# Kernel tuning notes

Measured on AMD Instinct MI355X. Metric: run time of the kernel, lower is better.

## Reference

```python
import jax, jax.numpy as jnp
import numpy as np

EPS = 1e-5
PATCH_HW = 4096   # 64*64
STEP = 2048


def _conv(x, w, b=None, stride=(1, 1), pad=((0, 0), (0, 0))):
    y = jax.lax.conv_general_dilated(x, w, stride, pad,
                                     dimension_numbers=('NCHW', 'OIHW', 'NCHW'))
    return y if b is None else y + b[None, :, None, None]


def _bn(x, s, b, m, v):
    # inference-mode BatchNorm2d
    inv = s * jax.lax.rsqrt(v + EPS)
    return (x - m[None, :, None, None]) * inv[None, :, None, None] + b[None, :, None, None]


def _forward(x, w1, b1, w2, b2, w3, b3,
             c5a_w, bn5a_s, bn5a_b, bn5a_m, bn5a_v,
             c5c_w, bn5c_s, bn5c_b, bn5c_m, bn5c_v,
             c51_w, bn51_s, bn51_b, bn51_m, bn51_v,
             c52_w, bn52_s, bn52_b, bn52_m, bn52_v,
             pam_q_w, pam_q_b, pam_k_w, pam_k_b, pam_v_w, pam_v_b,
             pam_gamma, cam_gamma, c8_w, c8_b):
    B, L = x.shape
    need = PATCH_HW - (L % PATCH_HW)          # torch pads even when L%hw==0; L chosen non-multiple
    xp = jnp.pad(x, ((0, 0), (0, need)))
    nw = (xp.shape[1] - PATCH_HW) // STEP + 1  # sliding windows (unfold)
    idx = jnp.arange(nw)[:, None] * STEP + jnp.arange(PATCH_HW)[None, :]
    # [nw,1,64,64].reshape(1,1,hw,nw) in torch is a pure row-major reshape
    c_in = xp[:, idx].reshape(B, 1, PATCH_HW, nw)   # [B,1,4096,61]
    # FCN backbone
    h = jax.nn.relu(_conv(c_in, w1, b1, (4, 4), ((4, 4), (4, 4))))   # [B,128,1025,16]
    h = jax.nn.relu(_conv(h, w2, b2, (2, 2), ((2, 2), (2, 2))))      # [B,256,513,8]
    h = jax.nn.relu(_conv(h, w3, b3, (1, 1), ((1, 1), (1, 1))))      # [B,128,513,8]
    p1 = ((1, 1), (1, 1))
    # PAM branch
    feat1 = jax.nn.relu(_bn(_conv(h, c5a_w, None, (1, 1), p1), bn5a_s, bn5a_b, bn5a_m, bn5a_v))
    _, C, Hh, Ww = feat1.shape
    N = Hh * Ww                                    # 4104
    q = _conv(feat1, pam_q_w, pam_q_b).reshape(B, -1, N)   # [B,4,N]
    k = _conv(feat1, pam_k_w, pam_k_b).reshape(B, -1, N)
    attn = jax.nn.softmax(jnp.einsum('bdn,bdm->bnm', q, k), axis=-1)   # [B,N,N], no scaling (as in source)
    v = _conv(feat1, pam_v_w, pam_v_b).reshape(B, C, N)
    sa = pam_gamma * jnp.einsum('bcj,bij->bci', v, attn).reshape(feat1.shape) + feat1
    sa_conv = jax.nn.relu(_bn(_conv(sa, c51_w, None, (1, 1), p1), bn51_s, bn51_b, bn51_m, bn51_v))
    # CAM branch
    feat2 = jax.nn.relu(_bn(_conv(h, c5c_w, None, (1, 1), p1), bn5c_s, bn5c_b, bn5c_m, bn5c_v))
    Xf = feat2.reshape(B, C, N)
    energy = jnp.einsum('bcn,bdn->bcd', Xf, Xf)                 # [B,C,C]
    cattn = jax.nn.softmax(jnp.max(energy, -1, keepdims=True) - energy, axis=-1)  # max-subtract inversion
    sc = cam_gamma * jnp.einsum('bcd,bdn->bcn', cattn, Xf).reshape(feat2.shape) + feat2
    sc_conv = jax.nn.relu(_bn(_conv(sc, c52_w, None, (1, 1), p1), bn52_s, bn52_b, bn52_m, bn52_v))
    # fused head output (conv8; dropout is identity in eval)
    out = _conv(sa_conv + sc_conv, c8_w, c8_b)                  # [B,nclass,513,8]
    return out[:, None]                                          # torch.stack adds a dim -> [B,1,nclass,513,8]


def setup_inputs() -> dict:
    key = jax.random.key(0)
    it = iter(jax.random.split(key, 40))
    def rn(shape, s=0.05):
        return jax.random.normal(next(it), shape, jnp.float32) * s
    d = {}
    d['x'] = jax.random.normal(next(it), (4, 126975), jnp.float32)
    d['w1'] = rn((128, 1, 8, 8));   d['b1'] = rn((128,))
    d['w2'] = rn((256, 128, 5, 5)); d['b2'] = rn((256,))
    d['w3'] = rn((128, 256, 3, 3)); d['b3'] = rn((128,))
    for tag, cin in (('5a', 128), ('5c', 128), ('51', 32), ('52', 32)):
        d['c' + tag + '_w'] = rn((32, cin, 3, 3))
        d['bn' + tag + '_s'] = jnp.ones((32,), jnp.float32)
        d['bn' + tag + '_b'] = jnp.zeros((32,), jnp.float32)
        d['bn' + tag + '_m'] = jnp.zeros((32,), jnp.float32)
        d['bn' + tag + '_v'] = jnp.ones((32,), jnp.float32)
    d['pam_q_w'] = rn((4, 32, 1, 1));  d['pam_q_b'] = rn((4,))
    d['pam_k_w'] = rn((4, 32, 1, 1));  d['pam_k_b'] = rn((4,))
    d['pam_v_w'] = rn((32, 32, 1, 1)); d['pam_v_b'] = rn((32,))
    d['pam_gamma'] = jnp.array([0.5], jnp.float32)  # nonzero so attention path is live
    d['cam_gamma'] = jnp.array([0.5], jnp.float32)
    d['c8_w'] = rn((2, 32, 1, 1)); d['c8_b'] = rn((2,))
    return d


def reference(x, w1, b1, w2, b2, w3, b3,
              c5a_w, bn5a_s, bn5a_b, bn5a_m, bn5a_v,
              c5c_w, bn5c_s, bn5c_b, bn5c_m, bn5c_v,
              c51_w, bn51_s, bn51_b, bn51_m, bn51_v,
              c52_w, bn52_s, bn52_b, bn52_m, bn52_v,
              pam_q_w, pam_q_b, pam_k_w, pam_k_b, pam_v_w, pam_v_b,
              pam_gamma, cam_gamma, c8_w, c8_b):
    return _forward(x, w1, b1, w2, b2, w3, b3,
                    c5a_w, bn5a_s, bn5a_b, bn5a_m, bn5a_v,
                    c5c_w, bn5c_s, bn5c_b, bn5c_m, bn5c_v,
                    c51_w, bn51_s, bn51_b, bn51_m, bn51_v,
                    c52_w, bn52_s, bn52_b, bn52_m, bn52_v,
                    pam_q_w, pam_q_b, pam_k_w, pam_k_b, pam_v_w, pam_v_b,
                    pam_gamma, cam_gamma, c8_w, c8_b)
```

## Files before the change

kernel.cpp:

```cpp
#include <hip/hip_runtime.h>
#include <cstddef>

constexpr int BB   = 4;
constexpr int LX   = 126975;
constexpr int H0   = 4096, W0 = 61;
constexpr int C1   = 128, H1 = 1025, W1 = 16;
constexpr int C2   = 256, H2 = 513,  W2 = 8;
constexpr int C3   = 128;
constexpr int NN   = H2 * W2;
constexpr int NSPLIT = 15;
constexpr int JSPAN  = 288;
constexpr int NPAD   = 4104;

constexpr size_t SZ_H1    = (size_t)BB * C1 * H1 * W1;
constexpr size_t SZ_P2    = (size_t)BB * C2 * NN;
constexpr size_t SZ_P3    = (size_t)BB * C3 * NN;
constexpr size_t SZ_F     = (size_t)BB * 32 * NN;
constexpr size_t SZ_QK    = (size_t)BB * 4 * NN;
constexpr size_t SZ_ACCP  = (size_t)NSPLIT * BB * 32 * NPAD;
constexpr size_t SZ_ML    = (size_t)NSPLIT * BB * 2 * NPAD;

constexpr size_t OFF_H1   = 0;
constexpr size_t OFF_P3A  = 0;
constexpr size_t OFF_P3B  = SZ_P3;
constexpr size_t OFF_ACCP = 0;
constexpr size_t OFF_ML   = OFF_ACCP + SZ_ACCP;
constexpr size_t RB       = SZ_H1;
constexpr size_t OFF_P2   = RB;
constexpr size_t OFF_F1   = RB;
constexpr size_t OFF_F2   = OFF_F1 + SZ_F;
constexpr size_t OFF_Q    = OFF_F2 + SZ_F;
constexpr size_t OFF_K    = OFF_Q  + SZ_QK;
constexpr size_t OFF_V    = OFF_K  + SZ_QK;
constexpr size_t OFF_SA   = OFF_V  + SZ_F;
constexpr size_t OFF_SC   = OFF_SA + SZ_F;
constexpr size_t OFF_EN   = RB + SZ_P2;
constexpr size_t OFF_W2T  = OFF_EN + 4096;
constexpr size_t OFF_W3T  = OFF_W2T + 819200;

__device__ __forceinline__ float frelu(float x) { return x > 0.f ? x : 0.f; }

__global__ __launch_bounds__(256) void k_wtrans(const float* __restrict__ w2,
                                                const float* __restrict__ w3,
                                                float* __restrict__ w2T,
                                                float* __restrict__ w3T) {
  const int k = blockIdx.x, oc = threadIdx.x;
  w2T[(size_t)k * 256 + oc] = w2[(size_t)oc * 3200 + k];
  if (k < 2304 && oc < 128) w3T[(size_t)k * 128 + oc] = w3[(size_t)oc * 2304 + k];
}

__global__ __launch_bounds__(256) void k_conv1(const float* __restrict__ x,
                                               const float* __restrict__ w1,
                                               const float* __restrict__ b1,
                                               float* __restrict__ h1) {
  __shared__ __align__(16) float tile[68 * 68];
  const int oh0 = blockIdx.x * 16;
  const int oc0 = blockIdx.y * 8;
  const int b   = blockIdx.z;
  const int tid = threadIdx.x;
  const int ih0 = oh0 * 4 - 4;
  for (int e = tid; e < 68 * 68; e += 256) {
    int row = e / 68, col = e - row * 68;
    int ih = ih0 + row, iw = col - 4;
    float v = 0.f;
    if (ih >= 0 && ih < H0 && iw >= 0 && iw < W0) {
      int l   = ih * W0 + iw;
      int pos = (l >> 12) * 2048 + (l & 4095);
      if (pos < LX) v = x[(size_t)b * LX + pos];
    }
    tile[e] = v;
  }
  __syncthreads();
  const int oh_l = tid >> 4, ow = tid & 15;
  float acc[8];
#pragma unroll
  for (int o = 0; o < 8; ++o) acc[o] = 0.f;
#pragma unroll
  for (int kh = 0; kh < 8; ++kh) {
    const float* rp = &tile[(4 * oh_l + kh) * 68 + 4 * ow];
    float4 a0 = *(const float4*)rp;
    float4 a1 = *(const float4*)(rp + 4);
    float r[8] = {a0.x, a0.y, a0.z, a0.w, a1.x, a1.y, a1.z, a1.w};
#pragma unroll
    for (int kw = 0; kw < 8; ++kw) {
#pragma unroll
      for (int o = 0; o < 8; ++o)
        acc[o] = fmaf(r[kw], w1[(oc0 + o) * 64 + kh * 8 + kw], acc[o]);
    }
  }
  const int oh = oh0 + oh_l;
  if (oh < H1) {
#pragma unroll
    for (int o = 0; o < 8; ++o) {
      float v = frelu(acc[o] + b1[oc0 + o]);
      h1[(((size_t)b * C1 + oc0 + o) * H1 + oh) * W1 + ow] = v;
    }
  }
}

__global__ __launch_bounds__(128) void k_conv2(const float* __restrict__ h1,
                                               const float* __restrict__ w2T,
                                               const float* __restrict__ b2,
                                               float* __restrict__ p2) {
  __shared__ __align__(16) float tin[4 * 19 * 20];
  const int oh0 = blockIdx.x * 8;
  const int oc0 = blockIdx.y * 32;
  const int b   = blockIdx.z;
  const int tid = threadIdx.x;
  const int oh_l = tid & 7, ocg = tid >> 3;
  const int ih0 = oh0 * 2 - 2;
  float acc[2][8] = {};
  for (int cc = 0; cc < 32; ++cc) {
    __syncthreads();
    for (int e = tid; e < 4 * 19 * 16; e += 128) {
      int ci = e / 304, r = e - ci * 304;
      int tr = r >> 4, c = r & 15;
      int ih = ih0 + tr;
      int cin = cc * 4 + ci;
      float v = 0.f;
      if (ih >= 0 && ih < H1) v = h1[(((size_t)b * C1 + cin) * H1 + ih) * W1 + c];
      tin[(ci * 19 + tr) * 20 + c] = v;
    }
    __syncthreads();
#pragma unroll 1
    for (int ci = 0; ci < 4; ++ci) {
      const float* wbase = &w2T[(size_t)((cc * 4 + ci) * 25) * 256 + oc0 + ocg * 2];
#pragma unroll
      for (int kh = 0; kh < 5; ++kh) {
        const float* rp = &tin[(ci * 19 + 2 * oh_l + kh) * 20];
        float4 a0 = *(const float4*)rp;
        float4 a1 = *(const float4*)(rp + 4);
        float4 a2 = *(const float4*)(rp + 8);
        float4 a3 = *(const float4*)(rp + 12);
        float rr[19];
        rr[0] = 0.f; rr[1] = 0.f; rr[18] = 0.f;
        rr[2] = a0.x; rr[3] = a0.y; rr[4] = a0.z; rr[5] = a0.w;
        rr[6] = a1.x; rr[7] = a1.y; rr[8] = a1.z; rr[9] = a1.w;
        rr[10] = a2.x; rr[11] = a2.y; rr[12] = a2.z; rr[13] = a2.w;
        rr[14] = a3.x; rr[15] = a3.y; rr[16] = a3.z; rr[17] = a3.w;
#pragma unroll
        for (int kw = 0; kw < 5; ++kw) {
          float2 wv = *(const float2*)&wbase[(kh * 5 + kw) * 256];
#pragma unroll
          for (int ow = 0; ow < 8; ++ow) {
            float r = rr[2 * ow + kw];
            acc[0][ow] = fmaf(r, wv.x, acc[0][ow]);
            acc[1][ow] = fmaf(r, wv.y, acc[1][ow]);
          }
        }
      }
    }
  }
  const int oh = oh0 + oh_l;
  if (oh < H2) {
#pragma unroll
    for (int o = 0; o < 2; ++o) {
      int oc = oc0 + ocg * 2 + o;
      float bo = b2[oc];
      float* dst = &p2[((size_t)b * C2 + oc) * NN + oh * 8];
      *(float4*)dst       = make_float4(frelu(acc[o][0] + bo), frelu(acc[o][1] + bo),
                                        frelu(acc[o][2] + bo), frelu(acc[o][3] + bo));
      *(float4*)(dst + 4) = make_float4(frelu(acc[o][4] + bo), frelu(acc[o][5] + bo),
                                        frelu(acc[o][6] + bo), frelu(acc[o][7] + bo));
    }
  }
}

__global__ __launch_bounds__(128) void k_conv3(const float* __restrict__ p2,
                                               const float* __restrict__ w3T,
                                               float* __restrict__ p3a,
                                               float* __restrict__ p3b) {
  __shared__ __align__(16) float tin[8 * 10 * 12];
  const int oh0  = blockIdx.x * 8;
  const int oc0  = (blockIdx.y & 3) * 32;
  const int half = blockIdx.y >> 2;
  const int b    = blockIdx.z;
  const int tid  = threadIdx.x;
  const int oh_l = tid & 7, ocg = tid >> 3;
  float acc[2][8] = {};
  float* outp = half ? p3b : p3a;
  for (int cc = 0; cc < 16; ++cc) {
    __syncthreads();
    for (int e = tid; e < 640; e += 128) {
      int ci = e / 80, r = e - ci * 80;
      int tr = r >> 3, c = r & 7;
      int ih = oh0 - 1 + tr;
      int cin = half * 128 + cc * 8 + ci;
      float v = 0.f;
      if (ih >= 0 && ih < H2) v = p2[((size_t)b * C2 + cin) * NN + ih * 8 + c];
      tin[(ci * 10 + tr) * 12 + c] = v;
    }
    __syncthreads();
#pragma unroll 1
    for (int ci = 0; ci < 8; ++ci) {
      const float* wbase = &w3T[(size_t)((half * 128 + cc * 8 + ci) * 9) * 128 + oc0 + ocg * 2];
#pragma unroll
      for (int kh = 0; kh < 3; ++kh) {
        const float* rp = &tin[(ci * 10 + oh_l + kh) * 12];
        float4 a0 = *(const float4*)rp;
        float4 a1 = *(const float4*)(rp + 4);
        float rr[10];
        rr[0] = 0.f; rr[9] = 0.f;
        rr[1] = a0.x; rr[2] = a0.y; rr[3] = a0.z; rr[4] = a0.w;
        rr[5] = a1.x; rr[6] = a1.y; rr[7] = a1.z; rr[8] = a1.w;
#pragma unroll
        for (int kw = 0; kw < 3; ++kw) {
          float2 wv = *(const float2*)&wbase[(kh * 3 + kw) * 128];
#pragma unroll
          for (int ow = 0; ow < 8; ++ow) {
            float r = rr[ow + kw];
            acc[0][ow] = fmaf(r, wv.x, acc[0][ow]);
            acc[1][ow] = fmaf(r, wv.y, acc[1][ow]);
          }
        }
      }
    }
  }
  const int oh = oh0 + oh_l;
  if (oh < H2) {
#pragma unroll
    for (int o = 0; o < 2; ++o) {
      int oc = oc0 + ocg * 2 + o;
      float* dst = &outp[((size_t)b * C3 + oc) * NN + oh * 8];
      *(float4*)dst       = make_float4(acc[o][0], acc[o][1], acc[o][2], acc[o][3]);
      *(float4*)(dst + 4) = make_float4(acc[o][4], acc[o][5], acc[o][6], acc[o][7]);
    }
  }
}

__global__ __launch_bounds__(128) void k_c5(const float* __restrict__ p3a,
                                            const float* __restrict__ p3b,
                                            const float* __restrict__ b3,
                                            const float* __restrict__ wa,
                                            const float* __restrict__ sa5, const float* __restrict__ ba5,
                                            const float* __restrict__ ma5, const float* __restrict__ va5,
                                            const float* __restrict__ wc,
                                            const float* __restrict__ sc5, const float* __restrict__ bc5,
                                            const float* __restrict__ mc5, const float* __restrict__ vc5,
                                            float* __restrict__ f1, float* __restrict__ f2) {
  __shared__ __align__(16) float tin[8 * 10 * 12];
  __shared__ __align__(16) float twt[72 * 64];
  const int oh0 = blockIdx.x * 8;
  const int b   = blockIdx.y;
  const int tid = threadIdx.x;
  const int vocg = tid >> 3, oh_l = tid & 7;
  float acc[4][8] = {};
  for (int cc = 0; cc < 16; ++cc) {
    __syncthreads();
    for (int e = tid; e < 640; e += 128) {
      int ci = e / 80, r = e - ci * 80;
      int tr = r >> 3, c = r & 7;
      int ih = oh0 - 1 + tr;
      int cin = cc * 8 + ci;
      float v = 0.f;
      if (ih >= 0 && ih < H2) {
        size_t idx = ((size_t)b * C3 + cin) * NN + ih * 8 + c;
        v = frelu(p3a[idx] + p3b[idx] + b3[cin]);
      }
      tin[(ci * 10 + tr) * 12 + c] = v;
    }
    for (int e = tid; e < 4608; e += 128) {
      int voc_l = e & 63, t = e >> 6;
      const float* base = (voc_l < 32) ? (wa + (size_t)voc_l * 1152) : (wc + (size_t)(voc_l - 32) * 1152);
      twt[t * 64 + voc_l] = base[cc * 8 * 9 + t];
    }
    __syncthreads();
#pragma unroll 1
    for (int ci = 0; ci < 8; ++ci) {
#pragma unroll
      for (int kh = 0; kh < 3; ++kh) {
        const float* rp = &tin[(ci * 10 + oh_l + kh) * 12];
        float4 a0 = *(const float4*)rp;
        float4 a1 = *(const float4*)(rp + 4);
        float rr[10];
        rr[0] = 0.f; rr[9] = 0.f;
        rr[1] = a0.x; rr[2] = a0.y; rr[3] = a0.z; rr[4] = a0.w;
        rr[5] = a1.x; rr[6] = a1.y; rr[7] = a1.z; rr[8] = a1.w;
#pragma unroll
        for (int kw = 0; kw < 3; ++kw) {
          float4 wv = *(const float4*)&twt[(ci * 9 + kh * 3 + kw) * 64 + vocg * 4];
#pragma unroll
          for (int ow = 0; ow < 8; ++ow) {
            float r = rr[ow + kw];
            acc[0][ow] = fmaf(r, wv.x, acc[0][ow]);
            acc[1][ow] = fmaf(r, wv.y, acc[1][ow]);
            acc[2][ow] = fmaf(r, wv.z, acc[2][ow]);
            acc[3][ow] = fmaf(r, wv.w, acc[3][ow]);
          }
        }
      }
    }
  }
  const int oh = oh0 + oh_l;
  if (oh < H2) {
#pragma unroll
    for (int vv = 0; vv < 4; ++vv) {
      int voc = vocg * 4 + vv;
      bool A = voc < 32;
      int ci = voc & 31;
      float sN = A ? sa5[ci] : sc5[ci];
      float bN = A ? ba5[ci] : bc5[ci];
      float mN = A ? ma5[ci] : mc5[ci];
      float vN = A ? va5[ci] : vc5[ci];
      float inv = sN * rsqrtf(vN + 1e-5f);
      float sh  = bN - mN * inv;
      float* dst = (A ? f1 : f2) + ((size_t)b * 32 + ci) * NN + oh * 8;
      float y[8];
#pragma unroll
      for (int ow = 0; ow < 8; ++ow) y[ow] = frelu(acc[vv][ow] * inv + sh);
      *(float4*)dst       = make_float4(y[0], y[1], y[2], y[3]);
      *(float4*)(dst + 4) = make_float4(y[4], y[5], y[6], y[7]);
    }
  }
}

__global__ __launch_bounds__(256) void k_qkv(const float* __restrict__ f1,
                                             const float* __restrict__ qw, const float* __restrict__ qbv,
                                             const float* __restrict__ kwp, const float* __restrict__ kbv,
                                             const float* __restrict__ vwp, const float* __restrict__ vbv,
                                             float* __restrict__ qo, float* __restrict__ ko,
                                             float* __restrict__ vo) {
  const int n = blockIdx.x * 256 + threadIdx.x;
  if (n >= NN) return;
  const int ocv = blockIdx.y, b = blockIdx.z;
  const float* w;
  float bias;
  float* dst;
  if (ocv < 4)      { w = qw + ocv * 32;        bias = qbv[ocv];     dst = qo + ((size_t)b * 4 + ocv) * NN; }
  else if (ocv < 8) { int o = ocv - 4; w = kwp + o * 32; bias = kbv[o]; dst = ko + ((size_t)b * 4 + o) * NN; }
  else              { int o = ocv - 8; w = vwp + o * 32; bias = vbv[o]; dst = vo + ((size_t)b * 32 + o) * NN; }
  float a = bias;
#pragma unroll
  for (int c = 0; c < 32; ++c) a = fmaf(f1[((size_t)b * 32 + c) * NN + n], w[c], a);
  dst[n] = a;
}

__device__ __forceinline__ float rmax32(const float (&p)[32]) {
  float x0 = p[0], x1 = p[1], x2 = p[2], x3 = p[3];
#pragma unroll
  for (int j = 4; j < 32; j += 4) {
    x0 = fmaxf(x0, p[j]); x1 = fmaxf(x1, p[j + 1]);
    x2 = fmaxf(x2, p[j + 2]); x3 = fmaxf(x3, p[j + 3]);
  }
  return fmaxf(fmaxf(x0, x1), fmaxf(x2, x3));
}
__device__ __forceinline__ float rsum32(const float (&p)[32]) {
  float x0 = p[0], x1 = p[1], x2 = p[2], x3 = p[3];
#pragma unroll
  for (int j = 4; j < 32; j += 4) { x0 += p[j]; x1 += p[j + 1]; x2 += p[j + 2]; x3 += p[j + 3]; }
  return (x0 + x1) + (x2 + x3);
}

__global__ __launch_bounds__(256) void k_flash(const float* __restrict__ qb,
                                               const float* __restrict__ kb,
                                               const float* __restrict__ vb,
                                               float* __restrict__ accp,
                                               float* __restrict__ mlb) {
  __shared__ __align__(16) float ks[4 * 32];
  __shared__ __align__(16) float vs[32 * 32];
  const int tid = threadIdx.x;
  const int ia  = blockIdx.x * 256 + tid;
  const int sp  = blockIdx.y;
  const int b   = blockIdx.z;
  float q[4];
#pragma unroll
  for (int d = 0; d < 4; ++d)
    q[d] = (ia < NN) ? qb[((size_t)b * 4 + d) * NN + ia] : 0.f;
  float m = -1e30f, l = 0.f;
  float acc[32];
#pragma unroll
  for (int c = 0; c < 32; ++c) acc[c] = 0.f;
  const int jbeg = sp * JSPAN;
  const int jend = (jbeg + JSPAN < NN) ? jbeg + JSPAN : NN;
  const int cs = tid >> 3, j4 = (tid & 7) * 4;
  for (int j0 = jbeg; j0 < jend; j0 += 32) {
    const int nv = (jend - j0 < 32) ? jend - j0 : 32;
    __syncthreads();
    {
      const float* vsrc = &vb[((size_t)b * 32 + cs) * NN + j0 + j4];
      float4 v4;
      if (j4 + 4 <= nv) {
        v4 = *(const float4*)vsrc;
      } else {
        v4.x = (j4 + 0 < nv) ? vsrc[0] : 0.f;
        v4.y = (j4 + 1 < nv) ? vsrc[1] : 0.f;
        v4.z = (j4 + 2 < nv) ? vsrc[2] : 0.f;
        v4.w = (j4 + 3 < nv) ? vsrc[3] : 0.f;
      }
      *(float4*)&vs[cs * 32 + j4] = v4;
      if (tid < 32) {
        const int d = tid >> 3;
        const float* ksrc = &kb[((size_t)b * 4 + d) * NN + j0 + j4];
        float4 k4;
        if (j4 + 4 <= nv) {
          k4 = *(const float4*)ksrc;
        } else {
          k4.x = (j4 + 0 < nv) ? ksrc[0] : 0.f;
          k4.y = (j4 + 1 < nv) ? ksrc[1] : 0.f;
          k4.z = (j4 + 2 < nv) ? ksrc[2] : 0.f;
          k4.w = (j4 + 3 < nv) ? ksrc[3] : 0.f;
        }
        *(float4*)&ks[d * 32 + j4] = k4;
      }
    }
    __syncthreads();
    float p[32];
#pragma unroll
    for (int jj = 0; jj < 8; ++jj) {
      float4 k0 = *(const float4*)&ks[0 * 32 + 4 * jj];
      float4 k1 = *(const float4*)&ks[1 * 32 + 4 * jj];
      float4 k2 = *(const float4*)&ks[2 * 32 + 4 * jj];
      float4 k3 = *(const float4*)&ks[3 * 32 + 4 * jj];
      p[4 * jj + 0] = fmaf(q[0], k0.x, fmaf(q[1], k1.x, fmaf(q[2], k2.x, q[3] * k3.x)));
      p[4 * jj + 1] = fmaf(q[0], k0.y, fmaf(q[1], k1.y, fmaf(q[2], k2.y, q[3] * k3.y)));
      p[4 * jj + 2] = fmaf(q[0], k0.z, fmaf(q[1], k1.z, fmaf(q[2], k2.z, q[3] * k3.z)));
      p[4 * jj + 3] = fmaf(q[0], k0.w, fmaf(q[1], k1.w, fmaf(q[2], k2.w, q[3] * k3.w)));
    }
    if (nv < 32) {
#pragma unroll
      for (int j = 0; j < 32; ++j)
        if (j >= nv) p[j] = -1e30f;
    }
    float mn = fmaxf(m, rmax32(p));
    float f = __expf(m - mn);
    m = mn;
#pragma unroll
    for (int j = 0; j < 32; ++j) p[j] = __expf(p[j] - mn);
    l = fmaf(l, f, rsum32(p));
#pragma unroll
    for (int c = 0; c < 32; ++c) acc[c] *= f;
#pragma unroll
    for (int jj = 0; jj < 8; ++jj) {
      float4 p4 = make_float4(p[4 * jj], p[4 * jj + 1], p[4 * jj + 2], p[4 * jj + 3]);
#pragma unroll
      for (int c = 0; c < 32; ++c) {
        float4 vv = *(const float4*)&vs[c * 32 + 4 * jj];
        acc[c] = fmaf(p4.x, vv.x, fmaf(p4.y, vv.y, fmaf(p4.z, vv.z, fmaf(p4.w, vv.w, acc[c]))));
      }
    }
  }
  if (ia < NN) {
    const size_t sb4 = (size_t)(sp * 4 + b);
#pragma unroll
    for (int c = 0; c < 32; ++c)
      accp[(sb4 * 32 + c) * NPAD + ia] = acc[c];
    mlb[(sb4 * 2 + 0) * NPAD + ia] = m;
    mlb[(sb4 * 2 + 1) * NPAD + ia] = l;
  }
}

__global__ __launch_bounds__(256) void k_combine(const float* __restrict__ accp,
                                                 const float* __restrict__ mlb,
                                                 const float* __restrict__ f1,
                                                 const float* __restrict__ gamma,
                                                 float* __restrict__ sa) {
  const int n = blockIdx.x * 256 + threadIdx.x;
  if (n >= NN) return;
  const int c = blockIdx.y, b = blockIdx.z;
  float m[NSPLIT], l[NSPLIT];
#pragma unroll
  for (int s = 0; s < NSPLIT; ++s) {
    m[s] = mlb[((size_t)(s * 4 + b) * 2 + 0) * NPAD + n];
    l[s] = mlb[((size_t)(s * 4 + b) * 2 + 1) * NPAD + n];
  }
  float ms = m[0];
#pragma unroll
  for (int s = 1; s < NSPLIT; ++s) ms = fmaxf(ms, m[s]);
  float den = 0.f, num = 0.f;
#pragma unroll
  for (int s = 0; s < NSPLIT; ++s) {
    float w = __expf(m[s] - ms);
    den = fmaf(l[s], w, den);
    num = fmaf(w, accp[((size_t)(s * 4 + b) * 32 + c) * NPAD + n], num);
  }
  size_t o = ((size_t)b * 32 + c) * NN + n;
  sa[o] = gamma[0] * num / den + f1[o];
}

__global__ __launch_bounds__(256) void k_zero(float* __restrict__ p) {
  int i = blockIdx.x * 256 + threadIdx.x;
  if (i < 4096) p[i] = 0.f;
}

__global__ __launch_bounds__(256) void k_energy(const float* __restrict__ f2,
                                                float* __restrict__ energy) {
  __shared__ float fs[32 * 257];
  const int n0 = blockIdx.x * 256, b = blockIdx.y, tid = threadIdx.x;
  for (int e = tid; e < 32 * 256; e += 256) {
    int c = e >> 8, nl = e & 255;
    int n = n0 + nl;
    fs[c * 257 + nl] = (n < NN) ? f2[((size_t)b * 32 + c) * NN + n] : 0.f;
  }
  __syncthreads();
  const int cg = tid >> 4, dg = tid & 15;
  const int c0 = cg * 2, d0 = dg * 2;
  float e00 = 0.f, e01 = 0.f, e10 = 0.f, e11 = 0.f;
  for (int t = 0; t < 256; ++t) {
    float a0 = fs[c0 * 257 + t], a1 = fs[(c0 + 1) * 257 + t];
    float b0 = fs[d0 * 257 + t], b1 = fs[(d0 + 1) * 257 + t];
    e00 = fmaf(a0, b0, e00); e01 = fmaf(a0, b1, e01);
    e10 = fmaf(a1, b0, e10); e11 = fmaf(a1, b1, e11);
  }
  float* eb = energy + b * 1024;
  atomicAdd(&eb[c0 * 32 + d0], e00);
  atomicAdd(&eb[c0 * 32 + d0 + 1], e01);
  atomicAdd(&eb[(c0 + 1) * 32 + d0], e10);
  atomicAdd(&eb[(c0 + 1) * 32 + d0 + 1], e11);
}

__global__ __launch_bounds__(64) void k_cam(const float* __restrict__ f2,
                                            const float* __restrict__ energy,
                                            const float* __restrict__ gamma,
                                            float* __restrict__ sc) {
  __shared__ __align__(16) float cat[32 * 32];
  const int lane = threadIdx.x, b = blockIdx.y;
  const int n = blockIdx.x * 64 + lane;
  if (lane < 32) {
    const float* eb = energy + b * 1024 + lane * 32;
    float e[32];
#pragma unroll
    for (int d = 0; d < 32; ++d) e[d] = eb[d];
    float mn = e[0];
#pragma unroll
    for (int d = 1; d < 32; ++d) mn = fminf(mn, e[d]);
    float w[32];
    float sum = 0.f;
#pragma unroll
    for (int d = 0; d < 32; ++d) { w[d] = __expf(mn - e[d]); sum += w[d]; }
    float inv = 1.f / sum;
#pragma unroll
    for (int d = 0; d < 32; ++d) cat[lane * 32 + d] = w[d] * inv;
  }
  __syncthreads();
  const bool ok = n < NN;
  float f[32];
#pragma unroll
  for (int c = 0; c < 32; ++c) f[c] = ok ? f2[((size_t)b * 32 + c) * NN + n] : 0.f;
  const float g = gamma[0];
#pragma unroll
  for (int c = 0; c < 32; ++c) {
    float a = 0.f;
#pragma unroll
    for (int k4 = 0; k4 < 8; ++k4) {
      float4 cw = *(const float4*)&cat[c * 32 + 4 * k4];
      a = fmaf(cw.x, f[4 * k4], fmaf(cw.y, f[4 * k4 + 1], fmaf(cw.z, f[4 * k4 + 2], fmaf(cw.w, f[4 * k4 + 3], a))));
    }
    if (ok) sc[((size_t)b * 32 + c) * NN + n] = g * a + f[c];
  }
}

__global__ __launch_bounds__(128) void k_final(const float* __restrict__ sa,
                                               const float* __restrict__ sc,
                                               const float* __restrict__ w51,
                                               const float* __restrict__ s51, const float* __restrict__ b51,
                                               const float* __restrict__ m51, const float* __restrict__ v51,
                                               const float* __restrict__ w52,
                                               const float* __restrict__ s52, const float* __restrict__ b52,
                                               const float* __restrict__ m52, const float* __restrict__ v52,
                                               const float* __restrict__ w8, const float* __restrict__ b8,
                                               float* __restrict__ out) {
  __shared__ __align__(16) float tin[2 * 8 * 10 * 12];
  __shared__ __align__(16) float twt[72 * 64];
  __shared__ float tmid[64 * 65];
  const int oh0 = blockIdx.x * 8;
  const int b   = blockIdx.y;
  const int tid = threadIdx.x;
  const int vocg = tid >> 3, oh_l = tid & 7;
  float acc[4][8] = {};
  for (int cc = 0; cc < 4; ++cc) {
    __syncthreads();
    for (int e = tid; e < 1280; e += 128) {
      int which = (e >= 640) ? 1 : 0;
      int r1 = e - which * 640;
      int ci = r1 / 80, r2 = r1 - ci * 80;
      int tr = r2 >> 3, c = r2 & 7;
      int ih = oh0 - 1 + tr;
      int cin = cc * 8 + ci;
      const float* src = which ? sc : sa;
      float v = 0.f;
      if (ih >= 0 && ih < H2) v = src[((size_t)b * 32 + cin) * NN + ih * 8 + c];
      tin[which * 960 + (ci * 10 + tr) * 12 + c] = v;
    }
    for (int e = tid; e < 4608; e += 128) {
      int voc_l = e & 63, t = e >> 6;
      const float* base = (voc_l < 32) ? (w51 + voc_l * 288) : (w52 + (voc_l - 32) * 288);
      twt[t * 64 + voc_l] = base[cc * 8 * 9 + t];
    }
    __syncthreads();
    const float* tbase = tin + (vocg < 8 ? 0 : 960);
#pragma unroll 1
    for (int ci = 0; ci < 8; ++ci) {
#pragma unroll
      for (int kh = 0; kh < 3; ++kh) {
        const float* rp = tbase + (ci * 10 + oh_l + kh) * 12;
        float4 a0 = *(const float4*)rp;
        float4 a1 = *(const float4*)(rp + 4);
        float rr[10];
        rr[0] = 0.f; rr[9] = 0.f;
        rr[1] = a0.x; rr[2] = a0.y; rr[3] = a0.z; rr[4] = a0.w;
        rr[5] = a1.x; rr[6] = a1.y; rr[7] = a1.z; rr[8] = a1.w;
#pragma unroll
        for (int kw = 0; kw < 3; ++kw) {
          float4 wv = *(const float4*)&twt[(ci * 9 + kh * 3 + kw) * 64 + vocg * 4];
#pragma unroll
          for (int ow = 0; ow < 8; ++ow) {
            float r = rr[ow + kw];
            acc[0][ow] = fmaf(r, wv.x, acc[0][ow]);
            acc[1][ow] = fmaf(r, wv.y, acc[1][ow]);
            acc[2][ow] = fmaf(r, wv.z, acc[2][ow]);
            acc[3][ow] = fmaf(r, wv.w, acc[3][ow]);
          }
        }
      }
    }
  }
  {
    float inv[4], sh[4];
#pragma unroll
    for (int vv = 0; vv < 4; ++vv) {
      int voc = vocg * 4 + vv;
      bool A = voc < 32;
      int ci = voc & 31;
      float sN = A ? s51[ci] : s52[ci];
      float bN = A ? b51[ci] : b52[ci];
      float mN = A ? m51[ci] : m52[ci];
      float vN = A ? v51[ci] : v52[ci];
      inv[vv] = sN * rsqrtf(vN + 1e-5f);
      sh[vv] = bN - mN * inv[vv];
    }
#pragma unroll
    for (int ow = 0; ow < 8; ++ow) {
      int pos = oh_l * 8 + ow;
#pragma unroll
      for (int vv = 0; vv < 4; ++vv) {
        float y = acc[vv][ow] * inv[vv] + sh[vv];
        tmid[pos * 65 + vocg * 4 + vv] = frelu(y);
      }
    }
  }
  __syncthreads();
  {
    const int o = tid >> 6, pos = tid & 63;
    const int oh = oh0 + (pos >> 3), ow = pos & 7;
    float a = b8[o];
    const float* wrow = w8 + o * 32;
#pragma unroll
    for (int c = 0; c < 32; ++c)
      a = fmaf(tmid[pos * 65 + c] + tmid[pos * 65 + 32 + c], wrow[c], a);
    if (oh < H2) out[((size_t)b * 2 + o) * NN + oh * 8 + ow] = a;
  }
}

extern "C" void kernel_launch(void* const* d_in, const int* in_sizes, int n_in,
                              void* d_out, int out_size, void* d_ws, size_t ws_size,
                              hipStream_t stream) {
  (void)in_sizes; (void)n_in; (void)out_size; (void)ws_size;
  const float* x      = (const float*)d_in[0];
  const float* w1     = (const float*)d_in[1];
  const float* b1     = (const float*)d_in[2];
  const float* w2     = (const float*)d_in[3];
  const float* b2     = (const float*)d_in[4];
  const float* w3     = (const float*)d_in[5];
  const float* b3     = (const float*)d_in[6];
  const float* c5a_w  = (const float*)d_in[7];
  const float* bn5a_s = (const float*)d_in[8];
  const float* bn5a_b = (const float*)d_in[9];
  const float* bn5a_m = (const float*)d_in[10];
  const float* bn5a_v = (const float*)d_in[11];
  const float* c5c_w  = (const float*)d_in[12];
  const float* bn5c_s = (const float*)d_in[13];
  const float* bn5c_b = (const float*)d_in[14];
  const float* bn5c_m = (const float*)d_in[15];
  const float* bn5c_v = (const float*)d_in[16];
  const float* c51_w  = (const float*)d_in[17];
  const float* bn51_s = (const float*)d_in[18];
  const float* bn51_b = (const float*)d_in[19];
  const float* bn51_m = (const float*)d_in[20];
  const float* bn51_v = (const float*)d_in[21];
  const float* c52_w  = (const float*)d_in[22];
  const float* bn52_s = (const float*)d_in[23];
  const float* bn52_b = (const float*)d_in[24];
  const float* bn52_m = (const float*)d_in[25];
  const float* bn52_v = (const float*)d_in[26];
  const float* pam_qw = (const float*)d_in[27];
  const float* pam_qb = (const float*)d_in[28];
  const float* pam_kw = (const float*)d_in[29];
  const float* pam_kb = (const float*)d_in[30];
  const float* pam_vw = (const float*)d_in[31];
  const float* pam_vb = (const float*)d_in[32];
  const float* pgamma = (const float*)d_in[33];
  const float* cgamma = (const float*)d_in[34];
  const float* c8_w   = (const float*)d_in[35];
  const float* c8_b   = (const float*)d_in[36];

  float* W    = (float*)d_ws;
  float* h1   = W + OFF_H1;
  float* p2   = W + OFF_P2;
  float* p3a  = W + OFF_P3A;
  float* p3b  = W + OFF_P3B;
  float* f1   = W + OFF_F1;
  float* f2   = W + OFF_F2;
  float* qbuf = W + OFF_Q;
  float* kbuf = W + OFF_K;
  float* vbuf = W + OFF_V;
  float* sab  = W + OFF_SA;
  float* scb  = W + OFF_SC;
  float* accp = W + OFF_ACCP;
  float* mlb  = W + OFF_ML;
  float* enb  = W + OFF_EN;
  float* w2T  = W + OFF_W2T;
  float* w3T  = W + OFF_W3T;
  float* outp = (float*)d_out;

  k_wtrans<<<dim3(3200), 256, 0, stream>>>(w2, w3, w2T, w3T);
  k_conv1<<<dim3(65, 16, 4), 256, 0, stream>>>(x, w1, b1, h1);
  k_conv2<<<dim3(65, 8, 4), 128, 0, stream>>>(h1, w2T, b2, p2);
  k_conv3<<<dim3(65, 8, 4), 128, 0, stream>>>(p2, w3T, p3a, p3b);
  k_c5<<<dim3(65, 4), 128, 0, stream>>>(p3a, p3b, b3,
                                        c5a_w, bn5a_s, bn5a_b, bn5a_m, bn5a_v,
                                        c5c_w, bn5c_s, bn5c_b, bn5c_m, bn5c_v,
                                        f1, f2);
  k_qkv<<<dim3(17, 40, 4), 256, 0, stream>>>(f1, pam_qw, pam_qb, pam_kw, pam_kb,
                                             pam_vw, pam_vb, qbuf, kbuf, vbuf);
  k_zero<<<dim3(16), 256, 0, stream>>>(enb);
  k_flash<<<dim3(17, NSPLIT, 4), 256, 0, stream>>>(qbuf, kbuf, vbuf, accp, mlb);
  k_energy<<<dim3(17, 4), 256, 0, stream>>>(f2, enb);
  k_combine<<<dim3(17, 32, 4), 256, 0, stream>>>(accp, mlb, f1, pgamma, sab);
  k_cam<<<dim3(65, 4), 64, 0, stream>>>(f2, enb, cgamma, scb);
  k_final<<<dim3(65, 4), 128, 0, stream>>>(sab, scb,
                                           c51_w, bn51_s, bn51_b, bn51_m, bn51_v,
                                           c52_w, bn52_s, bn52_b, bn52_m, bn52_v,
                                           c8_w, c8_b, outp);
}
```

Measured before the change: 1.563 ms.

## Run conv2 on bf16 MFMA with split hi/lo precision and channels-last input

After: 1.255 ms. -19.7%, faster.

```diff
diff --git a/kernel.cpp b/kernel.cpp
--- a/kernel.cpp
+++ b/kernel.cpp
@@ -20,7 +20,8 @@
 constexpr size_t SZ_ACCP  = (size_t)NSPLIT * BB * 32 * NPAD;
 constexpr size_t SZ_ML    = (size_t)NSPLIT * BB * 2 * NPAD;
 
-constexpr size_t OFF_H1   = 0;
+constexpr size_t OFF_H1CH = 0;
+constexpr size_t OFF_H1CL = 4198400;
 constexpr size_t OFF_P3A  = 0;
 constexpr size_t OFF_P3B  = SZ_P3;
 constexpr size_t OFF_ACCP = 0;
@@ -35,24 +36,46 @@
 constexpr size_t OFF_SA   = OFF_V  + SZ_F;
 constexpr size_t OFF_SC   = OFF_SA + SZ_F;
 constexpr size_t OFF_EN   = RB + SZ_P2;
-constexpr size_t OFF_W2T  = OFF_EN + 4096;
-constexpr size_t OFF_W3T  = OFF_W2T + 819200;
+constexpr size_t OFF_W2B  = OFF_EN + 4096;
+constexpr size_t OFF_W3T  = OFF_W2B + 819200;
 
 __device__ __forceinline__ float frelu(float x) { return x > 0.f ? x : 0.f; }
-
-__global__ __launch_bounds__(256) void k_wtrans(const float* __restrict__ w2,
-                                                const float* __restrict__ w3,
-                                                float* __restrict__ w2T,
-                                                float* __restrict__ w3T) {
+__device__ __forceinline__ ushort f2bf(float v) {
+  unsigned u = __float_as_uint(v);
+  return (ushort)((u + 0x7FFF + ((u >> 16) & 1)) >> 16);
+}
+
+typedef __attribute__((ext_vector_type(8))) short bf8;
+typedef __attribute__((ext_vector_type(4))) float f32x4;
+
+__global__ __launch_bounds__(128) void k_wcvt(const float* __restrict__ w2,
+                                              ushort* __restrict__ w2bh,
+                                              ushort* __restrict__ w2bl) {
+  const int oc = blockIdx.x, cin = threadIdx.x;
+  const float* src = w2 + (size_t)oc * 3200 + cin * 25;
+#pragma unroll 1
+  for (int p = 0; p < 25; ++p) {
+    float v = src[p];
+    ushort h = f2bf(v);
+    float hf = __uint_as_float(((unsigned)h) << 16);
+    ushort lo = f2bf(v - hf);
+    size_t o = ((size_t)p * 256 + oc) * 128 + cin;
+    w2bh[o] = h;
+    w2bl[o] = lo;
+  }
+}
+
+__global__ __launch_bounds__(128) void k_w3t(const float* __restrict__ w3,
+                                             float* __restrict__ w3T) {
   const int k = blockIdx.x, oc = threadIdx.x;
-  w2T[(size_t)k * 256 + oc] = w2[(size_t)oc * 3200 + k];
-  if (k < 2304 && oc < 128) w3T[(size_t)k * 128 + oc] = w3[(size_t)oc * 2304 + k];
+  w3T[(size_t)k * 128 + oc] = w3[(size_t)oc * 2304 + k];
 }
 
 __global__ __launch_bounds__(256) void k_conv1(const float* __restrict__ x,
                                                const float* __restrict__ w1,
                                                const float* __restrict__ b1,
-                                               float* __restrict__ h1) {
+                                               ushort* __restrict__ h1ch,
+                                               ushort* __restrict__ h1cl) {
   __shared__ __align__(16) float tile[68 * 68];
   const int oh0 = blockIdx.x * 16;
   const int oc0 = blockIdx.y * 8;
@@ -90,78 +113,100 @@
   }
   const int oh = oh0 + oh_l;
   if (oh < H1) {
-#pragma unroll
-    for (int o = 0; o < 8; ++o) {
-      float v = frelu(acc[o] + b1[oc0 + o]);
-      h1[(((size_t)b * C1 + oc0 + o) * H1 + oh) * W1 + ow] = v;
-    }
-  }
-}
-
-__global__ __launch_bounds__(128) void k_conv2(const float* __restrict__ h1,
-                                               const float* __restrict__ w2T,
+    unsigned hw[4], lw[4];
+#pragma unroll
+    for (int o2 = 0; o2 < 4; ++o2) {
+      float v0 = frelu(acc[2 * o2]     + b1[oc0 + 2 * o2]);
+      float v1 = frelu(acc[2 * o2 + 1] + b1[oc0 + 2 * o2 + 1]);
+      ushort h0 = f2bf(v0), h1u = f2bf(v1);
+      hw[o2] = (unsigned)h0 | ((unsigned)h1u << 16);
+      float l0 = v0 - __uint_as_float(((unsigned)h0) << 16);
+      float l1 = v1 - __uint_as_float(((unsigned)h1u) << 16);
+      lw[o2] = (unsigned)f2bf(l0) | ((unsigned)f2bf(l1) << 16);
+    }
+    size_t base = (((size_t)b * H1 + oh) * 16 + ow) * 128 + oc0;
+    *(uint4*)(h1ch + base) = make_uint4(hw[0], hw[1], hw[2], hw[3]);
+    *(uint4*)(h1cl + base) = make_uint4(lw[0], lw[1], lw[2], lw[3]);
+  }
+}
+
+__global__ __launch_bounds__(256) void k_conv2(const ushort* __restrict__ h1ch,
+                                               const ushort* __restrict__ h1cl,
+                                               const ushort* __restrict__ w2bh,
+                                               const ushort* __restrict__ w2bl,
                                                const float* __restrict__ b2,
                                                float* __restrict__ p2) {
-  __shared__ __align__(16) float tin[4 * 19 * 20];
-  const int oh0 = blockIdx.x * 8;
-  const int oc0 = blockIdx.y * 32;
-  const int b   = blockIdx.z;
-  const int tid = threadIdx.x;
-  const int oh_l = tid & 7, ocg = tid >> 3;
-  const int ih0 = oh0 * 2 - 2;
-  float acc[2][8] = {};
-  for (int cc = 0; cc < 32; ++cc) {
-    __syncthreads();
-    for (int e = tid; e < 4 * 19 * 16; e += 128) {
-      int ci = e / 304, r = e - ci * 304;
-      int tr = r >> 4, c = r & 15;
-      int ih = ih0 + tr;
-      int cin = cc * 4 + ci;
-      float v = 0.f;
-      if (ih >= 0 && ih < H1) v = h1[(((size_t)b * C1 + cin) * H1 + ih) * W1 + c];
-      tin[(ci * 19 + tr) * 20 + c] = v;
-    }
-    __syncthreads();
+  const int tid  = threadIdx.x;
+  const int lane = tid & 63, wid = tid >> 6;
+  const int row  = lane & 15, kg = lane >> 4;
+  const int b    = blockIdx.y;
+  const int mbase = blockIdx.x * 32;
+  int oh[2], ow[2];
+#pragma unroll
+  for (int mi = 0; mi < 2; ++mi) {
+    int mt = mbase + mi * 16 + row;
+    oh[mi] = mt >> 3;
+    ow[mi] = mt & 7;
+  }
+  const size_t bconst = (size_t)(wid * 64 + row) * 128 + 8 * kg;
+  const bf8 z = {0, 0, 0, 0, 0, 0, 0, 0};
+  f32x4 acc[2][4];
+#pragma unroll
+  for (int mi = 0; mi < 2; ++mi)
+#pragma unroll
+    for (int ns = 0; ns < 4; ++ns) acc[mi][ns] = (f32x4){0.f, 0.f, 0.f, 0.f};
 #pragma unroll 1
-    for (int ci = 0; ci < 4; ++ci) {
-      const float* wbase = &w2T[(size_t)((cc * 4 + ci) * 25) * 256 + oc0 + ocg * 2];
-#pragma unroll
-      for (int kh = 0; kh < 5; ++kh) {
-        const float* rp = &tin[(ci * 19 + 2 * oh_l + kh) * 20];
-        float4 a0 = *(const float4*)rp;
-        float4 a1 = *(const float4*)(rp + 4);
-        float4 a2 = *(const float4*)(rp + 8);
-        float4 a3 = *(const float4*)(rp + 12);
-        float rr[19];
-        rr[0] = 0.f; rr[1] = 0.f; rr[18] = 0.f;
-        rr[2] = a0.x; rr[3] = a0.y; rr[4] = a0.z; rr[5] = a0.w;
-        rr[6] = a1.x; rr[7] = a1.y; rr[8] = a1.z; rr[9] = a1.w;
-        rr[10] = a2.x; rr[11] = a2.y; rr[12] = a2.z; rr[13] = a2.w;
-        rr[14] = a3.x; rr[15] = a3.y; rr[16] = a3.z; rr[17] = a3.w;
-#pragma unroll
-        for (int kw = 0; kw < 5; ++kw) {
-          float2 wv = *(const float2*)&wbase[(kh * 5 + kw) * 256];
-#pragma unroll
-          for (int ow = 0; ow < 8; ++ow) {
-            float r = rr[2 * ow + kw];
-            acc[0][ow] = fmaf(r, wv.x, acc[0][ow]);
-            acc[1][ow] = fmaf(r, wv.y, acc[1][ow]);
+  for (int kh = 0; kh < 5; ++kh) {
+#pragma unroll 1
+    for (int kw = 0; kw < 5; ++kw) {
+      const int p = kh * 5 + kw;
+      const size_t bp = (size_t)p * 32768 + bconst;
+      bool ok[2];
+      size_t ab[2];
+#pragma unroll
+      for (int mi = 0; mi < 2; ++mi) {
+        int ih = 2 * oh[mi] + kh - 2;
+        int iw = 2 * ow[mi] + kw - 2;
+        ok[mi] = ((unsigned)ih < 1025u) && ((unsigned)iw < 16u);
+        ab[mi] = ok[mi] ? ((((size_t)b * 1025 + ih) * 16 + iw) * 128 + 8 * kg) : 0;
+      }
+#pragma unroll
+      for (int cc = 0; cc < 4; ++cc) {
+        bf8 ah[2], al[2];
+#pragma unroll
+        for (int mi = 0; mi < 2; ++mi) {
+          bf8 hv = *(const bf8*)(h1ch + ab[mi] + cc * 32);
+          bf8 lv = *(const bf8*)(h1cl + ab[mi] + cc * 32);
+          ah[mi] = ok[mi] ? hv : z;
+          al[mi] = ok[mi] ? lv : z;
+        }
+#pragma unroll
+        for (int ns = 0; ns < 4; ++ns) {
+          const size_t bo = bp + (size_t)ns * 2048 + cc * 32;
+          bf8 bh = *(const bf8*)(w2bh + bo);
+          bf8 bl = *(const bf8*)(w2bl + bo);
+#pragma unroll
+          for (int mi = 0; mi < 2; ++mi) {
+            acc[mi][ns] = __builtin_amdgcn_mfma_f32_16x16x32_bf16(ah[mi], bh, acc[mi][ns], 0, 0, 0);
+            acc[mi][ns] = __builtin_amdgcn_mfma_f32_16x16x32_bf16(ah[mi], bl, acc[mi][ns], 0, 0, 0);
+            acc[mi][ns] = __builtin_amdgcn_mfma_f32_16x16x32_bf16(al[mi], bh, acc[mi][ns], 0, 0, 0);
           }
         }
       }
     }
   }
-  const int oh = oh0 + oh_l;
-  if (oh < H2) {
-#pragma unroll
-    for (int o = 0; o < 2; ++o) {
-      int oc = oc0 + ocg * 2 + o;
-      float bo = b2[oc];
-      float* dst = &p2[((size_t)b * C2 + oc) * NN + oh * 8];
-      *(float4*)dst       = make_float4(frelu(acc[o][0] + bo), frelu(acc[o][1] + bo),
-                                        frelu(acc[o][2] + bo), frelu(acc[o][3] + bo));
-      *(float4*)(dst + 4) = make_float4(frelu(acc[o][4] + bo), frelu(acc[o][5] + bo),
-                                        frelu(acc[o][6] + bo), frelu(acc[o][7] + bo));
+#pragma unroll
+  for (int mi = 0; mi < 2; ++mi) {
+    const int m0 = mbase + mi * 16 + kg * 4;
+    if (m0 < NN) {
+#pragma unroll
+      for (int ns = 0; ns < 4; ++ns) {
+        const int oc = wid * 64 + ns * 16 + row;
+        const float bo = b2[oc];
+        float* dst = &p2[((size_t)b * C2 + oc) * NN + m0];
+        *(float4*)dst = make_float4(frelu(acc[mi][ns][0] + bo), frelu(acc[mi][ns][1] + bo),
+                                    frelu(acc[mi][ns][2] + bo), frelu(acc[mi][ns][3] + bo));
+      }
     }
   }
 }
@@ -694,7 +739,8 @@
   const float* c8_b   = (const float*)d_in[36];
 
   float* W    = (float*)d_ws;
-  float* h1   = W + OFF_H1;
+  ushort* h1ch = (ushort*)(W + OFF_H1CH);
+  ushort* h1cl = (ushort*)(W + OFF_H1CL);
   float* p2   = W + OFF_P2;
   float* p3a  = W + OFF_P3A;
   float* p3b  = W + OFF_P3B;
@@ -708,13 +754,15 @@
   float* accp = W + OFF_ACCP;
   float* mlb  = W + OFF_ML;
   float* enb  = W + OFF_EN;
-  float* w2T  = W + OFF_W2T;
+  ushort* w2bh = (ushort*)(W + OFF_W2B);
+  ushort* w2bl = (ushort*)(W + OFF_W2B + 409600);
   float* w3T  = W + OFF_W3T;
   float* outp = (float*)d_out;
 
-  k_wtrans<<<dim3(3200), 256, 0, stream>>>(w2, w3, w2T, w3T);
-  k_conv1<<<dim3(65, 16, 4), 256, 0, stream>>>(x, w1, b1, h1);
-  k_conv2<<<dim3(65, 8, 4), 128, 0, stream>>>(h1, w2T, b2, p2);
+  k_wcvt<<<dim3(256), 128, 0, stream>>>(w2, w2bh, w2bl);
+  k_w3t<<<dim3(2304), 128, 0, stream>>>(w3, w3T);
+  k_conv1<<<dim3(65, 16, 4), 256, 0, stream>>>(x, w1, b1, h1ch, h1cl);
+  k_conv2<<<dim3(129, 4), 256, 0, stream>>>(h1ch, h1cl, w2bh, w2bl, b2, p2);
   k_conv3<<<dim3(65, 8, 4), 128, 0, stream>>>(p2, w3T, p3a, p3b);
   k_c5<<<dim3(65, 4), 128, 0, stream>>>(p3a, p3b, b3,
                                         c5a_w, bn5a_s, bn5a_b, bn5a_m, bn5a_v,
```
